# Kernel optimization log

Measured on AMD Instinct MI355X. Metric: run time of the kernel, lower is better.

Reference implementation:

```python
import jax, jax.numpy as jnp
from jax import lax
import numpy as np

WS = 8      # window_size
SS = 4      # shift_size
NH = 8      # num_heads
DIM = 192
HID = int(DIM * 2.66)  # 510


def _rel_pos_index(ws):
    coords = np.stack(np.meshgrid(np.arange(ws), np.arange(ws), indexing='ij'))
    flat = coords.reshape(2, -1)
    rel = (flat[:, :, None] - flat[:, None, :]).transpose(1, 2, 0)
    rel[..., 0] += ws - 1
    rel[..., 1] += ws - 1
    rel[..., 0] *= 2 * ws - 1
    return rel.sum(-1)  # (ws*ws, ws*ws) int


def _attn_mask(Hp, Wp, ws, ss):
    img = np.zeros((Hp, Wp), dtype=np.float32)
    slices = (slice(0, -ws), slice(-ws, -ss), slice(-ss, None))
    cnt = 0
    for h in slices:
        for w in slices:
            img[h, w] = cnt
            cnt += 1
    mw = img.reshape(Hp // ws, ws, Wp // ws, ws).transpose(0, 2, 1, 3).reshape(-1, ws * ws)
    am = mw[:, None, :] - mw[:, :, None]
    return np.where(am != 0, -100.0, 0.0).astype(np.float32)  # (nW, N, N)


def _ln(t, w, b):
    mu = t.mean(-1, keepdims=True)
    var = t.var(-1, keepdims=True)
    return (t - mu) / jnp.sqrt(var + 1e-5) * w + b


def setup_inputs() -> dict:
    key = jax.random.key(0)
    ks = jax.random.split(key, 12)
    s = 0.05
    return {
        'x': jax.random.normal(ks[0], (2, DIM, 256, 256), jnp.float32),
        'norm1_w': jnp.ones((DIM,), jnp.float32),
        'norm1_b': jnp.zeros((DIM,), jnp.float32),
        'qkv_w': jax.random.normal(ks[1], (3 * DIM, DIM), jnp.float32) * s,
        'rpb_table': jax.random.normal(ks[2], ((2 * WS - 1) * (2 * WS - 1), NH), jnp.float32) * 0.02,
        'proj_w': jax.random.normal(ks[3], (DIM, DIM), jnp.float32) * s,
        'proj_b': jnp.zeros((DIM,), jnp.float32),
        'norm2_w': jnp.ones((DIM,), jnp.float32),
        'norm2_b': jnp.zeros((DIM,), jnp.float32),
        'pin_w': jax.random.normal(ks[4], (2 * HID, DIM), jnp.float32) * s,
        'dw_w': jax.random.normal(ks[5], (2 * HID, 1, 3, 3), jnp.float32) * s,
        'pout_w': jax.random.normal(ks[6], (DIM, HID), jnp.float32) * s,
    }


def reference(x, norm1_w, norm1_b, qkv_w, rpb_table, proj_w, proj_b,
              norm2_w, norm2_b, pin_w, dw_w, pout_w):
    B, C, H, W = x.shape
    hd = C // NH
    scale = hd ** -0.5

    # ---- norm1 (channel-last layernorm) ----
    xc = jnp.transpose(x, (0, 2, 3, 1))  # BHWC
    xn = _ln(xc, norm1_w, norm1_b)

    # ---- pad to window multiple ----
    pad_b = (WS - H % WS) % WS
    pad_r = (WS - W % WS) % WS
    xn = jnp.pad(xn, ((0, 0), (0, pad_b), (0, pad_r), (0, 0)))
    Hp, Wp = H + pad_b, W + pad_r

    # ---- cyclic shift ----
    sx = jnp.roll(xn, (-SS, -SS), axis=(1, 2))

    # ---- window partition ----
    nH, nW = Hp // WS, Wp // WS
    N = WS * WS
    xw = sx.reshape(B, nH, WS, nW, WS, C).transpose(0, 1, 3, 2, 4, 5)
    xw = xw.reshape(B * nH * nW, N, C)

    # ---- window attention ----
    qkv = (xw @ qkv_w.T).reshape(-1, N, 3, NH, hd).transpose(2, 0, 3, 1, 4)
    q, k, v = qkv[0] * scale, qkv[1], qkv[2]  # (B_, NH, N, hd)
    attn = jnp.einsum('bhnd,bhmd->bhnm', q, k)

    idx = _rel_pos_index(WS)
    bias = rpb_table[idx.reshape(-1)].reshape(N, N, NH).transpose(2, 0, 1)
    attn = attn + bias[None]

    mask = jnp.asarray(_attn_mask(Hp, Wp, WS, SS))  # (nWtot, N, N)
    nWtot = nH * nW
    attn = attn.reshape(B, nWtot, NH, N, N) + mask[None, :, None]
    attn = jax.nn.softmax(attn.reshape(-1, NH, N, N), axis=-1)

    out = jnp.einsum('bhnm,bhmd->bhnd', attn, v)
    out = out.transpose(0, 2, 1, 3).reshape(-1, N, C)
    out = out @ proj_w.T + proj_b

    # ---- window reverse + unshift + crop ----
    out = out.reshape(B, nH, nW, WS, WS, C).transpose(0, 1, 3, 2, 4, 5)
    out = out.reshape(B, Hp, Wp, C)
    out = jnp.roll(out, (SS, SS), axis=(1, 2))[:, :H, :W]
    x = x + jnp.transpose(out, (0, 3, 1, 2))

    # ---- FFN: 1x1 in -> depthwise 3x3 -> gated gelu -> 1x1 out ----
    y = _ln(jnp.transpose(x, (0, 2, 3, 1)), norm2_w, norm2_b)
    y = jnp.transpose(y, (0, 3, 1, 2))
    y = jnp.einsum('bchw,oc->bohw', y, pin_w)
    y = lax.conv_general_dilated(y, dw_w, (1, 1), 'SAME',
                                 feature_group_count=dw_w.shape[0],
                                 dimension_numbers=('NCHW', 'OIHW', 'NCHW'))
    h = dw_w.shape[0] // 2
    y = jax.nn.gelu(y[:, :h], approximate=False) * y[:, h:]
    y = jnp.einsum('bchw,oc->bohw', y, pout_w)
    return x + y
```

## Files before the change

### kernel.cpp

```cpp
#include <hip/hip_runtime.h>
#include <hip/hip_bf16.h>
#include <math.h>

#define CDIM 192
#define NTOK 131072
#define HD 24
#define NHEADS 8
#define NTC 65536

typedef __attribute__((ext_vector_type(4))) float floatx4;
typedef __attribute__((ext_vector_type(8))) short bf16x8;
typedef __attribute__((ext_vector_type(4))) unsigned int uintx4;

static __device__ __forceinline__ float bf2f(__hip_bfloat16 h) { return __bfloat162float(h); }
static __device__ __forceinline__ __hip_bfloat16 f2bf(float f) { return __float2bfloat16(f); }
static __device__ __forceinline__ float s2f(short s) {
  union { unsigned u; float f; } c; c.u = ((unsigned)(unsigned short)s) << 16; return c.f;
}
static __device__ __forceinline__ short f2s(float f) {
  __hip_bfloat16 h = __float2bfloat16(f);
  union { __hip_bfloat16 h; short s; } c; c.h = h; return c.s;
}
static __device__ __forceinline__ void load_lds16(const void* g, void* l) {
  __builtin_amdgcn_global_load_lds(
      (const __attribute__((address_space(1))) void*)g,
      (__attribute__((address_space(3))) void*)l, 16, 0, 0);
}

__global__ __launch_bounds__(256) void kcvt(
    const float* __restrict__ in, __hip_bfloat16* __restrict__ out, int n) {
  int i = blockIdx.x * 256 + threadIdx.x;
  if (i < n) out[i] = f2bf(in[i]);
}

__global__ __launch_bounds__(256) void k0_padpout(
    const float* __restrict__ w, __hip_bfloat16* __restrict__ o) {
  int idx = blockIdx.x * 256 + threadIdx.x;
  int n = idx >> 9, k = idx & 511;
  o[idx] = (k < 510) ? f2bf(w[n * 510 + k]) : f2bf(0.f);
}

__global__ __launch_bounds__(256) void k0_padpin(
    const float* __restrict__ w, const float* __restrict__ nw,
    __hip_bfloat16* __restrict__ o) {
  int idx = blockIdx.x * 256 + threadIdx.x;
  int n = idx / 192, k = idx % 192;
  int src = (n < 510) ? n : ((n >= 512 && n < 1022) ? n - 2 : -1);
  o[idx] = (src >= 0) ? f2bf(w[src * 192 + k] * nw[k]) : f2bf(0.f);
}

__global__ __launch_bounds__(256) void k0_st(
    const float* __restrict__ w, const float* __restrict__ nw,
    const float* __restrict__ nb, float* __restrict__ S, float* __restrict__ T) {
  int n = blockIdx.x * 256 + threadIdx.x;
  int src = (n < 510) ? n : ((n >= 512 && n < 1022) ? n - 2 : -1);
  float s = 0.f, t = 0.f;
  if (src >= 0)
    for (int c = 0; c < 192; ++c) {
      float v = w[src * 192 + c];
      s += v * nw[c]; t += v * nb[c];
    }
  S[n] = s; T[n] = t;
}

__global__ __launch_bounds__(256) void k0_wtap(
    const float* __restrict__ wdw, __hip_bfloat16* __restrict__ wa,
    __hip_bfloat16* __restrict__ wg) {
  int idx = blockIdx.x * 256 + threadIdx.x;
  if (idx >= 9 * 512) return;
  int tap = idx >> 9, c = idx & 511;
  wa[idx] = (c < 510) ? f2bf(wdw[c * 9 + tap]) : f2bf(0.f);
  wg[idx] = (c < 510) ? f2bf(wdw[(c + 510) * 9 + tap]) : f2bf(0.f);
}

__global__ __launch_bounds__(256) void k1_ln_raster(
    const float* __restrict__ x,
    const float* __restrict__ w,
    const float* __restrict__ bsh,
    __hip_bfloat16* __restrict__ out) {
  __shared__ float xs[32][193];
  __shared__ float wls[192], bls[192];
  int bid = blockIdx.x;
  int b = bid >> 11, si = (bid >> 3) & 255, sj0 = (bid & 7) << 5;
  int i = (si + 4) & 255;
  int tid = threadIdx.x;
  int lane = tid & 63, wv = tid >> 6;
  if (tid < 192) { wls[tid] = w[tid]; bls[tid] = bsh[tid]; }
  int p0 = (lane & 7) << 2;
  int cb = wv * 8 + (lane >> 3);
  int j4 = (sj0 + p0 + 4) & 255;
  long pbase = ((long)(b * CDIM + cb) << 16) + (i << 8) + j4;
  #pragma unroll
  for (int co = 0; co < 6; ++co) {
    floatx4 v = *(const floatx4*)(x + pbase + ((long)co << 21));
    int c = co * 32 + cb;
    xs[p0 + 0][c] = v[0];
    xs[p0 + 1][c] = v[1];
    xs[p0 + 2][c] = v[2];
    xs[p0 + 3][c] = v[3];
  }
  __syncthreads();
  int p = tid >> 3, q = tid & 7, c0 = q * 24;
  float v[24], s = 0.f, sq = 0.f;
  #pragma unroll
  for (int e = 0; e < 24; ++e) {
    float t = xs[p][c0 + e]; v[e] = t; s += t; sq += t * t;
  }
  #pragma unroll
  for (int off = 1; off < 8; off <<= 1) { s += __shfl_xor(s, off); sq += __shfl_xor(sq, off); }
  float mean = s * (1.0f / 192.0f);
  float var  = sq * (1.0f / 192.0f) - mean * mean;
  float rstd = rsqrtf(var + 1e-5f);
  unsigned pk[12];
  #pragma unroll
  for (int e = 0; e < 12; ++e) {
    unsigned lo = (unsigned short)f2s((v[2*e  ] - mean) * rstd * wls[c0 + 2*e  ] + bls[c0 + 2*e  ]);
    unsigned hi = (unsigned short)f2s((v[2*e+1] - mean) * rstd * wls[c0 + 2*e+1] + bls[c0 + 2*e+1]);
    pk[e] = lo | (hi << 16);
  }
  long tok0 = ((long)b << 16) + (si << 8) + sj0;
  char* gout = (char*)out + (tok0 + p) * 384 + q * 48;
  *(uintx4*)(gout     ) = (uintx4){pk[0], pk[1], pk[2], pk[3]};
  *(uintx4*)(gout + 16) = (uintx4){pk[4], pk[5], pk[6], pk[7]};
  *(uintx4*)(gout + 32) = (uintx4){pk[8], pk[9], pk[10], pk[11]};
}

template <int WM, int WN, int EPI>
__global__ __launch_bounds__(256) void gemm_lds(
    const __hip_bfloat16* __restrict__ A,
    const __hip_bfloat16* __restrict__ B,
    const float* __restrict__ bias,
    __hip_bfloat16* __restrict__ C,
    int K, int lda, int ldb, int ldc) {
  constexpr int BM = 32 * WM, BN = 32 * WN;
  __shared__ __hip_bfloat16 As[BM * 32];
  __shared__ __hip_bfloat16 Bs[BN * 32];
  int t = threadIdx.x;
  int wave = t >> 6, lane = t & 63;
  int wm = wave >> 1, wn = wave & 1;
  int r16 = lane & 15, quad = lane >> 4;
  long m0 = (long)blockIdx.y * BM;
  long n0 = (long)blockIdx.x * BN;
  int srow = t >> 2, scol = (t & 3) << 3;
  floatx4 acc[WM][WN];
  for (int i = 0; i < WM; ++i)
    for (int j = 0; j < WN; ++j)
      acc[i][j] = (floatx4){0.f, 0.f, 0.f, 0.f};
  for (int k0 = 0; k0 < K; k0 += 32) {
    __syncthreads();
    for (int p = 0; p < WM / 2; ++p)
      load_lds16(A + (m0 + srow + p * 64) * lda + k0 + scol,
                 (char*)As + t * 16 + p * 4096);
    for (int p = 0; p < WN / 2; ++p)
      load_lds16(B + (n0 + srow + p * 64) * ldb + k0 + scol,
                 (char*)Bs + t * 16 + p * 4096);
    __syncthreads();
    bf16x8 af[WM], bf[WN];
    for (int i = 0; i < WM; ++i)
      af[i] = *(const bf16x8*)&As[(wm * 16 * WM + i * 16 + r16) * 32 + quad * 8];
    for (int j = 0; j < WN; ++j)
      bf[j] = *(const bf16x8*)&Bs[(wn * 16 * WN + j * 16 + r16) * 32 + quad * 8];
    for (int i = 0; i < WM; ++i)
      for (int j = 0; j < WN; ++j)
        acc[i][j] = __builtin_amdgcn_mfma_f32_16x16x32_bf16(af[i], bf[j], acc[i][j], 0, 0, 0);
  }
  for (int i = 0; i < WM; ++i)
    for (int j = 0; j < WN; ++j) {
      int col = n0 + wn * 16 * WN + j * 16 + r16;
      float badd = (EPI == 1) ? bias[col] : 0.f;
      for (int r = 0; r < 4; ++r) {
        long row = m0 + wm * 16 * WM + i * 16 + quad * 4 + r;
        C[row * ldc + col] = f2bf(acc[i][j][r] + badd);
      }
    }
}

__global__ __launch_bounds__(256) void gemm_qkv(
    const __hip_bfloat16* __restrict__ A,
    const __hip_bfloat16* __restrict__ B,
    __hip_bfloat16* __restrict__ C) {
  constexpr int WM = 4, WN = 2, BM = 128, BN = 64;
  __shared__ __hip_bfloat16 As[BM * 32];
  __shared__ __hip_bfloat16 Bs[BN * 32];
  int t = threadIdx.x;
  int wave = t >> 6, lane = t & 63;
  int wm = wave >> 1, wn = wave & 1;
  int r16 = lane & 15, quad = lane >> 4;
  long m0 = (long)blockIdx.y * BM;
  int n0 = blockIdx.x * BN;
  int srow = t >> 2, scol = (t & 3) << 3;
  floatx4 acc[WM][WN];
  for (int i = 0; i < WM; ++i)
    for (int j = 0; j < WN; ++j)
      acc[i][j] = (floatx4){0.f, 0.f, 0.f, 0.f};
  for (int k0 = 0; k0 < 192; k0 += 32) {
    __syncthreads();
    for (int p = 0; p < 2; ++p)
      load_lds16(A + (m0 + srow + p * 64) * 192 + k0 + scol,
                 (char*)As + t * 16 + p * 4096);
    load_lds16(B + (n0 + srow) * 192 + k0 + scol, (char*)Bs + t * 16);
    __syncthreads();
    bf16x8 af[WM], bf[WN];
    for (int i = 0; i < WM; ++i)
      af[i] = *(const bf16x8*)&As[(wm * 64 + i * 16 + r16) * 32 + quad * 8];
    for (int j = 0; j < WN; ++j)
      bf[j] = *(const bf16x8*)&Bs[(wn * 32 + j * 16 + r16) * 32 + quad * 8];
    for (int i = 0; i < WM; ++i)
      for (int j = 0; j < WN; ++j)
        acc[i][j] = __builtin_amdgcn_mfma_f32_16x16x32_bf16(af[i], bf[j], acc[i][j], 0, 0, 0);
  }
  for (int i = 0; i < WM; ++i)
    for (int j = 0; j < WN; ++j) {
      int col = n0 + wn * 32 + j * 16 + r16;
      int sel = col / 192;
      int cm = col - sel * 192;
      int h = (cm * 683) >> 14;
      int d = cm - h * 24;
      long cb = (long)sel * (NTC * 256) + ((long)h << 21) + d;
      for (int r = 0; r < 4; ++r) {
        long row = m0 + wm * 64 + i * 16 + quad * 4 + r;
        C[cb + (row << 5)] = f2bf(acc[i][j][r]);
      }
    }
}

__global__ __launch_bounds__(256) void gemm_pin(
    const __hip_bfloat16* __restrict__ x2,
    const __hip_bfloat16* __restrict__ B,
    const float* __restrict__ stats,
    const float* __restrict__ Sv,
    const float* __restrict__ Tv,
    __hip_bfloat16* __restrict__ C,
    int bb, int r0) {
  constexpr int WM = 4, WN = 4, BM = 128, BN = 128;
  __shared__ __hip_bfloat16 As[BM * 32];
  __shared__ __hip_bfloat16 Bs[BN * 32];
  int t = threadIdx.x;
  int wave = t >> 6, lane = t & 63;
  int wm = wave >> 1, wn = wave & 1;
  int r16 = lane & 15, quad = lane >> 4;
  int m0 = blockIdx.y * BM;
  int n0 = blockIdx.x * BN;
  int srow = t >> 2, scol = (t & 3) << 3;
  floatx4 acc[WM][WN];
  for (int i = 0; i < WM; ++i)
    for (int j = 0; j < WN; ++j)
      acc[i][j] = (floatx4){0.f, 0.f, 0.f, 0.f};
  for (int k0 = 0; k0 < 192; k0 += 32) {
    __syncthreads();
    for (int p = 0; p < 2; ++p) {
      int rr = m0 + srow + p * 64;
      int il = rr >> 8, jj = rr & 255;
      int gi = r0 - 1 + il; gi = gi < 0 ? 0 : (gi > 255 ? 255 : gi);
      long tok = ((long)bb << 16) + (gi << 8) + jj;
      load_lds16(x2 + tok * 192 + k0 + scol, (char*)As + t * 16 + p * 4096);
    }
    for (int p = 0; p < 2; ++p)
      load_lds16(B + (n0 + srow + p * 64) * 192 + k0 + scol,
                 (char*)Bs + t * 16 + p * 4096);
    __syncthreads();
    bf16x8 af[WM], bf[WN];
    for (int i = 0; i < WM; ++i)
      af[i] = *(const bf16x8*)&As[(wm * 64 + i * 16 + r16) * 32 + quad * 8];
    for (int j = 0; j < WN; ++j)
      bf[j] = *(const bf16x8*)&Bs[(wn * 64 + j * 16 + r16) * 32 + quad * 8];
    for (int i = 0; i < WM; ++i)
      for (int j = 0; j < WN; ++j)
        acc[i][j] = __builtin_amdgcn_mfma_f32_16x16x32_bf16(af[i], bf[j], acc[i][j], 0, 0, 0);
  }
  for (int i = 0; i < WM; ++i) {
    float mr[4], rsd[4];
    #pragma unroll
    for (int r = 0; r < 4; ++r) {
      int row = m0 + wm * 64 + i * 16 + quad * 4 + r;
      int il = row >> 8, jj = row & 255;
      int gi = r0 - 1 + il; gi = gi < 0 ? 0 : (gi > 255 ? 255 : gi);
      long tok = ((long)bb << 16) + (gi << 8) + jj;
      mr[r] = stats[2 * tok]; rsd[r] = stats[2 * tok + 1];
    }
    for (int j = 0; j < WN; ++j) {
      int col = n0 + wn * 64 + j * 16 + r16;
      float sv = Sv[col], tv = Tv[col];
      for (int r = 0; r < 4; ++r) {
        int row = m0 + wm * 64 + i * 16 + quad * 4 + r;
        C[(long)row * 1024 + col] = f2bf(acc[i][j][r] * rsd[r] - mr[r] * rsd[r] * sv + tv);
      }
    }
  }
}

__global__ __launch_bounds__(256) void gemm_pout(
    const __hip_bfloat16* __restrict__ A,
    const __hip_bfloat16* __restrict__ B,
    const __hip_bfloat16* __restrict__ x2,
    float* __restrict__ out,
    int b, int r0) {
  constexpr int WM = 2, WN = 4, BM = 64, BN = 128;
  __shared__ __hip_bfloat16 As[BM * 32];
  __shared__ __hip_bfloat16 Bs[BN * 32];
  int t = threadIdx.x;
  int wave = t >> 6, lane = t & 63;
  int wm = wave >> 1, wn = wave & 1;
  int r16 = lane & 15, quad = lane >> 4;
  long m0 = (long)blockIdx.y * BM;
  long n0 = (long)blockIdx.x * BN;
  int srow = t >> 2, scol = (t & 3) << 3;
  floatx4 acc[WM][WN];
  for (int i = 0; i < WM; ++i)
    for (int j = 0; j < WN; ++j)
      acc[i][j] = (floatx4){0.f, 0.f, 0.f, 0.f};
  for (int k0 = 0; k0 < 512; k0 += 32) {
    __syncthreads();
    load_lds16(A + (m0 + srow) * 512 + k0 + scol, (char*)As + t * 16);
    for (int p = 0; p < WN / 2; ++p)
      load_lds16(B + (n0 + srow + p * 64) * 512 + k0 + scol,
                 (char*)Bs + t * 16 + p * 4096);
    __syncthreads();
    bf16x8 af[WM], bf[WN];
    for (int i = 0; i < WM; ++i)
      af[i] = *(const bf16x8*)&As[(wm * 16 * WM + i * 16 + r16) * 32 + quad * 8];
    for (int j = 0; j < WN; ++j)
      bf[j] = *(const bf16x8*)&Bs[(wn * 16 * WN + j * 16 + r16) * 32 + quad * 8];
    for (int i = 0; i < WM; ++i)
      for (int j = 0; j < WN; ++j)
        acc[i][j] = __builtin_amdgcn_mfma_f32_16x16x32_bf16(af[i], bf[j], acc[i][j], 0, 0, 0);
  }
  for (int i = 0; i < WM; ++i)
    for (int j = 0; j < WN; ++j) {
      int p_ = n0 + wn * 16 * WN + j * 16 + r16;
      int il = p_ >> 8, jj = p_ & 255;
      long pix = ((long)(r0 + il) << 8) + jj;
      for (int r = 0; r < 4; ++r) {
        int c_ = m0 + wm * 16 * WM + i * 16 + quad * 4 + r;
        long tok = ((long)b << 16) + pix;
        float v = acc[i][j][r] + bf2f(x2[tok * CDIM + c_]);
        out[((long)(b * CDIM + c_) << 16) + pix] = v;
      }
    }
}

__global__ __launch_bounds__(256) void k3_attn(
    const __hip_bfloat16* __restrict__ qkv,
    const float* __restrict__ rpb,
    __hip_bfloat16* __restrict__ out,
    int wid0) {
  __shared__ alignas(16) short Kp[64 * 32];
  __shared__ alignas(16) short Vt[32 * 64];
  __shared__ alignas(16) short Ps[4][16 * 64];
  __shared__ float rpbs[225];
  int h = blockIdx.x, widl = blockIdx.y;
  int wid = wid0 + widl;
  int t = threadIdx.x;
  int wv = t >> 6, lane = t & 63, quad = lane >> 4, r16 = lane & 15;
  int wi_l = widl >> 5, wjl = widl & 31;
  const short* qk = (const short*)qkv;
  const short* Qp  = qk + ((long)h << 21);
  const short* Kpg = Qp + (long)NTC * 256;
  const short* Vpg = Qp + (long)NTC * 512;

  if (t < 225) rpbs[t] = rpb[t * NHEADS + h];

  {
    int kr = t >> 2, kq = t & 3;
    bf16x8 kv = {0, 0, 0, 0, 0, 0, 0, 0};
    if (kq < 3) {
      int ltok = ((((wi_l << 3) + (kr >> 3)) << 8) + (wjl << 3) + (kr & 7));
      kv = *(const bf16x8*)(Kpg + ((long)ltok << 5) + kq * 8);
    }
    *(bf16x8*)&Kp[kr * 32 + ((kq ^ ((kr >> 1) & 3)) << 3)] = kv;
  }
  {
    int tok = t & 63, q8 = t >> 6;
    if (q8 < 3) {
      int ltok = ((((wi_l << 3) + (tok >> 3)) << 8) + (wjl << 3) + (tok & 7));
      bf16x8 vv = *(const bf16x8*)(Vpg + ((long)ltok << 5) + q8 * 8);
      #pragma unroll
      for (int e = 0; e < 8; ++e) {
        int d = q8 * 8 + e;
        Vt[d * 64 + (((tok >> 3) ^ (d & 7)) << 3) + (tok & 7)] = vv[e];
      }
    } else {
      int zt = t - 192;
      int d = 24 + (zt >> 3), tokg = zt & 7;
      bf16x8 z = {0, 0, 0, 0, 0, 0, 0, 0};
      *(bf16x8*)&Vt[d * 64 + ((tokg ^ (d & 7)) << 3)] = z;
    }
  }
  bf16x8 qf = {0, 0, 0, 0, 0, 0, 0, 0};
  if (quad < 3) {
    int nn = wv * 16 + r16;
    int ltok = ((((wi_l << 3) + (nn >> 3)) << 8) + (wjl << 3) + (nn & 7));
    qf = *(const bf16x8*)(Qp + ((long)ltok << 5) + quad * 8);
  }
  __syncthreads();

  floatx4 sj[4];
  int kswz = (quad ^ ((r16 >> 1) & 3)) << 3;
  #pragma unroll
  for (int j = 0; j < 4; ++j) {
    bf16x8 kf = *(const bf16x8*)&Kp[(j * 16 + r16) * 32 + kswz];
    sj[j] = __builtin_amdgcn_mfma_f32_16x16x32_bf16(
        qf, kf, (floatx4){0.f, 0.f, 0.f, 0.f}, 0, 0, 0);
  }

  int b = wid >> 10, wi = (wid >> 5) & 31, wj = wid & 31;
  int rkj[4];
  #pragma unroll
  for (int j = 0; j < 4; ++j) {
    int m = j * 16 + r16;
    int gsi = wi * 8 + (m >> 3), gsj = wj * 8 + (m & 7);
    rkj[j] = ((gsi < 248) ? 0 : (gsi < 252 ? 1 : 2)) * 3 +
             ((gsj < 248) ? 0 : (gsj < 252 ? 1 : 2));
  }

  float rs[4];
  #pragma unroll
  for (int r = 0; r < 4; ++r) {
    int n = wv * 16 + quad * 4 + r;
    int ti = n >> 3, tj = n & 7;
    int gi = wi * 8 + ti, gj = wj * 8 + tj;
    int rq = ((gi < 248) ? 0 : (gi < 252 ? 1 : 2)) * 3 +
             ((gj < 248) ? 0 : (gj < 252 ? 1 : 2));
    float val[4];
    float mx = -1e30f;
    #pragma unroll
    for (int j = 0; j < 4; ++j) {
      int m = j * 16 + r16;
      int idx = (ti - (m >> 3) + 7) * 15 + (tj - (m & 7) + 7);
      float v = sj[j][r] * 0.20412414523193154f + rpbs[idx];
      if (rkj[j] != rq) v -= 100.0f;
      val[j] = v;
      mx = fmaxf(mx, v);
    }
    #pragma unroll
    for (int off = 1; off < 16; off <<= 1) mx = fmaxf(mx, __shfl_xor(mx, off));
    float sum = 0.f;
    int row = quad * 4 + r;
    #pragma unroll
    for (int j = 0; j < 4; ++j) {
      float p = __expf(val[j] - mx);
      sum += p;
      int col = j * 16 + r16;
      Ps[wv][row * 64 + ((((col >> 3) ^ (row & 7)) << 3)) + (col & 7)] = f2s(p);
    }
    #pragma unroll
    for (int off = 1; off < 16; off <<= 1) sum += __shfl_xor(sum, off);
    rs[r] = 1.0f / sum;
  }
  __syncthreads();

  floatx4 o0 = {0.f, 0.f, 0.f, 0.f}, o1 = {0.f, 0.f, 0.f, 0.f};
  #pragma unroll
  for (int kk = 0; kk < 2; ++kk) {
    int g = (((kk * 4 + quad) ^ (r16 & 7)) << 3);
    bf16x8 pa = *(const bf16x8*)&Ps[wv][r16 * 64 + g];
    bf16x8 b0 = *(const bf16x8*)&Vt[r16 * 64 + g];
    bf16x8 b1 = *(const bf16x8*)&Vt[(16 + r16) * 64 + g];
    o0 = __builtin_amdgcn_mfma_f32_16x16x32_bf16(pa, b0, o0, 0, 0, 0);
    o1 = __builtin_amdgcn_mfma_f32_16x16x32_bf16(pa, b1, o1, 0, 0, 0);
  }
  #pragma unroll
  for (int r = 0; r < 4; ++r) {
    int n = wv * 16 + quad * 4 + r;
    int gi = wi * 8 + (n >> 3), gj = wj * 8 + (n & 7);
    long ob = (((long)b << 16) + (gi << 8) + gj) * CDIM + h * HD;
    out[ob + r16] = f2bf(o0[r] * rs[r]);
    if (r16 < 8) out[ob + 16 + r16] = f2bf(o1[r] * rs[r]);
  }
}

__global__ __launch_bounds__(256) void k4_res_raster(
    const float* __restrict__ x,
    const __hip_bfloat16* __restrict__ tmp,
    __hip_bfloat16* __restrict__ x2,
    float* __restrict__ stats) {
  __shared__ float xs[32][193];
  int bid = blockIdx.x;
  int b = bid >> 11, i = (bid >> 3) & 255, j0 = (bid & 7) << 5;
  int tid = threadIdx.x;
  int lane = tid & 63, wv = tid >> 6;
  int p0 = (lane & 7) << 2;
  int cb = wv * 8 + (lane >> 3);
  long pbase = ((long)(b * CDIM + cb) << 16) + (i << 8) + j0 + p0;
  #pragma unroll
  for (int co = 0; co < 6; ++co) {
    floatx4 v = *(const floatx4*)(x + pbase + ((long)co << 21));
    int c = co * 32 + cb;
    xs[p0 + 0][c] = v[0];
    xs[p0 + 1][c] = v[1];
    xs[p0 + 2][c] = v[2];
    xs[p0 + 3][c] = v[3];
  }
  __syncthreads();
  int p = tid >> 3, q = tid & 7, c0 = q * 24;
  int j = j0 + p;
  int si = (i + 252) & 255, sj = (j + 252) & 255;
  long tsh = ((long)b << 16) + (si << 8) + sj;
  const short* tp = (const short*)tmp + tsh * 192 + c0;
  bf16x8 t0 = *(const bf16x8*)(tp);
  bf16x8 t1 = *(const bf16x8*)(tp + 8);
  bf16x8 t2v = *(const bf16x8*)(tp + 16);
  float v[24], s = 0.f, sq = 0.f;
  #pragma unroll
  for (int e = 0; e < 8; ++e) {
    float a0 = xs[p][c0 + e     ] + s2f(t0[e]);
    float a1 = xs[p][c0 + e + 8 ] + s2f(t1[e]);
    float a2 = xs[p][c0 + e + 16] + s2f(t2v[e]);
    v[e] = a0; v[e + 8] = a1; v[e + 16] = a2;
    s += a0 + a1 + a2;
    sq += a0 * a0 + a1 * a1 + a2 * a2;
  }
  #pragma unroll
  for (int off = 1; off < 8; off <<= 1) { s += __shfl_xor(s, off); sq += __shfl_xor(sq, off); }
  float mean = s * (1.0f / 192.0f);
  float var  = sq * (1.0f / 192.0f) - mean * mean;
  float rstd = rsqrtf(var + 1e-5f);
  long t2g = ((long)b << 16) + (i << 8) + j;
  if (q == 0) { stats[2 * t2g] = mean; stats[2 * t2g + 1] = rstd; }
  unsigned pk[12];
  #pragma unroll
  for (int e = 0; e < 12; ++e) {
    unsigned lo = (unsigned short)f2s(v[2 * e]);
    unsigned hi = (unsigned short)f2s(v[2 * e + 1]);
    pk[e] = lo | (hi << 16);
  }
  char* gout = (char*)x2 + t2g * 384 + q * 48;
  *(uintx4*)(gout     ) = (uintx4){pk[0], pk[1], pk[2], pk[3]};
  *(uintx4*)(gout + 16) = (uintx4){pk[4], pk[5], pk[6], pk[7]};
  *(uintx4*)(gout + 32) = (uintx4){pk[8], pk[9], pk[10], pk[11]};
}

__global__ __launch_bounds__(256) void k7_dwgate(
    const __hip_bfloat16* __restrict__ pin,
    const __hip_bfloat16* __restrict__ wa,
    const __hip_bfloat16* __restrict__ wg,
    __hip_bfloat16* __restrict__ out,
    int r0) {
  int t = threadIdx.x;
  int oct = t & 63, pl = t >> 6;
  int p = blockIdx.x * 4 + pl;
  int il = p >> 8, j = p & 255;
  int gi = r0 + il;
  int c0 = oct << 3;
  float a[8], g[8];
  for (int e = 0; e < 8; ++e) { a[e] = 0.f; g[e] = 0.f; }
  for (int di = -1; di <= 1; ++di) {
    int ii = gi + di; if (ii < 0 || ii > 255) continue;
    int br = il + di + 1;
    for (int dj = -1; dj <= 1; ++dj) {
      int jj = j + dj; if (jj < 0 || jj > 255) continue;
      long nbase = ((long)((br << 8) + jj)) << 10;
      int tap = (di + 1) * 3 + (dj + 1);
      bf16x8 va  = *(const bf16x8*)((const short*)pin + nbase + c0);
      bf16x8 vg  = *(const bf16x8*)((const short*)pin + nbase + 512 + c0);
      bf16x8 wa8 = *(const bf16x8*)((const short*)wa + tap * 512 + c0);
      bf16x8 wg8 = *(const bf16x8*)((const short*)wg + tap * 512 + c0);
      for (int e = 0; e < 8; ++e) {
        a[e] += s2f(wa8[e]) * s2f(va[e]);
        g[e] += s2f(wg8[e]) * s2f(vg[e]);
      }
    }
  }
  bf16x8 r;
  for (int e = 0; e < 8; ++e) {
    float ge = 0.5f * a[e] * (1.0f + erff(a[e] * 0.70710678118654752f));
    r[e] = f2s(ge * g[e]);
  }
  *(bf16x8*)((short*)out + (long)p * 512 + c0) = r;
}

extern "C" void kernel_launch(void* const* d_in, const int* in_sizes, int n_in,
                              void* d_out, int out_size, void* d_ws, size_t ws_size,
                              hipStream_t stream) {
  const float* x       = (const float*)d_in[0];
  const float* norm1_w = (const float*)d_in[1];
  const float* norm1_b = (const float*)d_in[2];
  const float* qkv_w   = (const float*)d_in[3];
  const float* rpb     = (const float*)d_in[4];
  const float* proj_w  = (const float*)d_in[5];
  const float* proj_b  = (const float*)d_in[6];
  const float* norm2_w = (const float*)d_in[7];
  const float* norm2_b = (const float*)d_in[8];
  const float* pin_w   = (const float*)d_in[9];
  const float* dw_w    = (const float*)d_in[10];
  const float* pout_w  = (const float*)d_in[11];

  char* ws = (char*)d_ws;
  __hip_bfloat16* wsLN1 = (__hip_bfloat16*)(ws);
  __hip_bfloat16* wsPRJ = (__hip_bfloat16*)(ws);
  __hip_bfloat16* wsPINC= (__hip_bfloat16*)(ws);
  __hip_bfloat16* wsATT = (__hip_bfloat16*)(ws + 50331648UL);
  __hip_bfloat16* wsX2  = (__hip_bfloat16*)(ws + 50331648UL);
  float*          wsST  = (float*)         (ws + 100663296UL);
  __hip_bfloat16* wsGT  = (__hip_bfloat16*)(ws + 101711872UL);
  __hip_bfloat16* wsWA  = (__hip_bfloat16*)(ws + 118489088UL);
  __hip_bfloat16* wsWG  = (__hip_bfloat16*)(ws + 118507520UL);
  float*          wsS   = (float*)         (ws + 118517760UL);
  float*          wsT   = (float*)         (ws + 118525952UL);
  __hip_bfloat16* wsPW  = (__hip_bfloat16*)(ws + 120586240UL);
  __hip_bfloat16* wsQW  = (__hip_bfloat16*)(ws + 120782848UL);
  __hip_bfloat16* wsPJW = (__hip_bfloat16*)(ws + 121004032UL);
  __hip_bfloat16* wsPIW = (__hip_bfloat16*)(ws + 121077760UL);
  float* out = (float*)d_out;
  __hip_bfloat16* qkvbuf = (__hip_bfloat16*)d_out;

  kcvt<<<(110592 + 255) / 256, 256, 0, stream>>>(qkv_w, wsQW, 110592);
  kcvt<<<(36864 + 255) / 256, 256, 0, stream>>>(proj_w, wsPJW, 36864);
  k0_padpout<<<384, 256, 0, stream>>>(pout_w, wsPW);
  k0_padpin<<<768, 256, 0, stream>>>(pin_w, norm2_w, wsPIW);
  k0_st<<<4, 256, 0, stream>>>(pin_w, norm2_w, norm2_b, wsS, wsT);
  k0_wtap<<<18, 256, 0, stream>>>(dw_w, wsWA, wsWG);
  k1_ln_raster<<<4096, 256, 0, stream>>>(x, norm1_w, norm1_b, wsLN1);
  for (int b = 0; b < 2; ++b) {
    gemm_qkv<<<dim3(9, 512), 256, 0, stream>>>(
        wsLN1 + (long)b * 65536 * CDIM, wsQW, qkvbuf);
    k3_attn<<<dim3(8, 1024), 256, 0, stream>>>(qkvbuf, rpb, wsATT, b * 1024);
  }
  gemm_lds<4, 2, 1><<<dim3(3, 1024), 256, 0, stream>>>(
      wsATT, wsPJW, proj_b, wsPRJ, 192, 192, 192, 192);
  k4_res_raster<<<4096, 256, 0, stream>>>(x, wsPRJ, wsX2, wsST);
  for (int cc = 0; cc < 8; ++cc) {
    int b = cc >> 2, r0 = (cc & 3) * 64;
    gemm_pin<<<dim3(8, 132), 256, 0, stream>>>(
        wsX2, wsPIW, wsST, wsS, wsT, wsPINC, b, r0);
    k7_dwgate<<<4096, 256, 0, stream>>>(wsPINC, wsWA, wsWG, wsGT, r0);
    gemm_pout<<<dim3(128, 3), 256, 0, stream>>>(wsPW, wsGT, wsX2, out, b, r0);
  }
}
```

Measured before the change: 929.7 us.

## Store QKV token-major via generic GEMM and group attention blocks by window

Drops the custom QKV GEMM that scattered output into a head-major padded layout. The generic GEMM now writes a plain token-major 576-wide row, and the attention kernel reads Q/K/V slices at per-head offsets. The attention grid becomes 1D, with blocks remapped so the eight heads of a group of windows run next to each other for better cache locality. The GEMM stores become contiguous, but attention loads now use a larger stride (48-byte pieces out of 1152-byte rows).

```diff
diff --git a/kernel.cpp b/kernel.cpp
--- a/kernel.cpp
+++ b/kernel.cpp
@@ -175,55 +175,6 @@
     }
 }
 
-__global__ __launch_bounds__(256) void gemm_qkv(
-    const __hip_bfloat16* __restrict__ A,
-    const __hip_bfloat16* __restrict__ B,
-    __hip_bfloat16* __restrict__ C) {
-  constexpr int WM = 4, WN = 2, BM = 128, BN = 64;
-  __shared__ __hip_bfloat16 As[BM * 32];
-  __shared__ __hip_bfloat16 Bs[BN * 32];
-  int t = threadIdx.x;
-  int wave = t >> 6, lane = t & 63;
-  int wm = wave >> 1, wn = wave & 1;
-  int r16 = lane & 15, quad = lane >> 4;
-  long m0 = (long)blockIdx.y * BM;
-  int n0 = blockIdx.x * BN;
-  int srow = t >> 2, scol = (t & 3) << 3;
-  floatx4 acc[WM][WN];
-  for (int i = 0; i < WM; ++i)
-    for (int j = 0; j < WN; ++j)
-      acc[i][j] = (floatx4){0.f, 0.f, 0.f, 0.f};
-  for (int k0 = 0; k0 < 192; k0 += 32) {
-    __syncthreads();
-    for (int p = 0; p < 2; ++p)
-      load_lds16(A + (m0 + srow + p * 64) * 192 + k0 + scol,
-                 (char*)As + t * 16 + p * 4096);
-    load_lds16(B + (n0 + srow) * 192 + k0 + scol, (char*)Bs + t * 16);
-    __syncthreads();
-    bf16x8 af[WM], bf[WN];
-    for (int i = 0; i < WM; ++i)
-      af[i] = *(const bf16x8*)&As[(wm * 64 + i * 16 + r16) * 32 + quad * 8];
-    for (int j = 0; j < WN; ++j)
-      bf[j] = *(const bf16x8*)&Bs[(wn * 32 + j * 16 + r16) * 32 + quad * 8];
-    for (int i = 0; i < WM; ++i)
-      for (int j = 0; j < WN; ++j)
-        acc[i][j] = __builtin_amdgcn_mfma_f32_16x16x32_bf16(af[i], bf[j], acc[i][j], 0, 0, 0);
-  }
-  for (int i = 0; i < WM; ++i)
-    for (int j = 0; j < WN; ++j) {
-      int col = n0 + wn * 32 + j * 16 + r16;
-      int sel = col / 192;
-      int cm = col - sel * 192;
-      int h = (cm * 683) >> 14;
-      int d = cm - h * 24;
-      long cb = (long)sel * (NTC * 256) + ((long)h << 21) + d;
-      for (int r = 0; r < 4; ++r) {
-        long row = m0 + wm * 64 + i * 16 + quad * 4 + r;
-        C[cb + (row << 5)] = f2bf(acc[i][j][r]);
-      }
-    }
-}
-
 __global__ __launch_bounds__(256) void gemm_pin(
     const __hip_bfloat16* __restrict__ x2,
     const __hip_bfloat16* __restrict__ B,
@@ -348,15 +299,14 @@
   __shared__ alignas(16) short Vt[32 * 64];
   __shared__ alignas(16) short Ps[4][16 * 64];
   __shared__ float rpbs[225];
-  int h = blockIdx.x, widl = blockIdx.y;
+  int bidx = blockIdx.x;
+  int h = (bidx >> 3) & 7;
+  int widl = ((bidx >> 6) << 3) | (bidx & 7);
   int wid = wid0 + widl;
   int t = threadIdx.x;
   int wv = t >> 6, lane = t & 63, quad = lane >> 4, r16 = lane & 15;
   int wi_l = widl >> 5, wjl = widl & 31;
   const short* qk = (const short*)qkv;
-  const short* Qp  = qk + ((long)h << 21);
-  const short* Kpg = Qp + (long)NTC * 256;
-  const short* Vpg = Qp + (long)NTC * 512;
 
   if (t < 225) rpbs[t] = rpb[t * NHEADS + h];
 
@@ -364,16 +314,16 @@
     int kr = t >> 2, kq = t & 3;
     bf16x8 kv = {0, 0, 0, 0, 0, 0, 0, 0};
     if (kq < 3) {
-      int ltok = ((((wi_l << 3) + (kr >> 3)) << 8) + (wjl << 3) + (kr & 7));
-      kv = *(const bf16x8*)(Kpg + ((long)ltok << 5) + kq * 8);
+      long ltok = (long)((((wi_l << 3) + (kr >> 3)) << 8) + (wjl << 3) + (kr & 7));
+      kv = *(const bf16x8*)(qk + ltok * 576 + 192 + h * HD + kq * 8);
     }
     *(bf16x8*)&Kp[kr * 32 + ((kq ^ ((kr >> 1) & 3)) << 3)] = kv;
   }
   {
     int tok = t & 63, q8 = t >> 6;
     if (q8 < 3) {
-      int ltok = ((((wi_l << 3) + (tok >> 3)) << 8) + (wjl << 3) + (tok & 7));
-      bf16x8 vv = *(const bf16x8*)(Vpg + ((long)ltok << 5) + q8 * 8);
+      long ltok = (long)((((wi_l << 3) + (tok >> 3)) << 8) + (wjl << 3) + (tok & 7));
+      bf16x8 vv = *(const bf16x8*)(qk + ltok * 576 + 384 + h * HD + q8 * 8);
       #pragma unroll
       for (int e = 0; e < 8; ++e) {
         int d = q8 * 8 + e;
@@ -389,8 +339,8 @@
   bf16x8 qf = {0, 0, 0, 0, 0, 0, 0, 0};
   if (quad < 3) {
     int nn = wv * 16 + r16;
-    int ltok = ((((wi_l << 3) + (nn >> 3)) << 8) + (wjl << 3) + (nn & 7));
-    qf = *(const bf16x8*)(Qp + ((long)ltok << 5) + quad * 8);
+    long ltok = (long)((((wi_l << 3) + (nn >> 3)) << 8) + (wjl << 3) + (nn & 7));
+    qf = *(const bf16x8*)(qk + ltok * 576 + h * HD + quad * 8);
   }
   __syncthreads();
 
@@ -612,9 +562,9 @@
   k0_wtap<<<18, 256, 0, stream>>>(dw_w, wsWA, wsWG);
   k1_ln_raster<<<4096, 256, 0, stream>>>(x, norm1_w, norm1_b, wsLN1);
   for (int b = 0; b < 2; ++b) {
-    gemm_qkv<<<dim3(9, 512), 256, 0, stream>>>(
-        wsLN1 + (long)b * 65536 * CDIM, wsQW, qkvbuf);
-    k3_attn<<<dim3(8, 1024), 256, 0, stream>>>(qkvbuf, rpb, wsATT, b * 1024);
+    gemm_lds<4, 2, 0><<<dim3(9, 512), 256, 0, stream>>>(
+        wsLN1 + (long)b * 65536 * CDIM, wsQW, nullptr, qkvbuf, 192, 192, 192, 576);
+    k3_attn<<<8192, 256, 0, stream>>>(qkvbuf, rpb, wsATT, b * 1024);
   }
   gemm_lds<4, 2, 1><<<dim3(3, 1024), 256, 0, stream>>>(
       wsATT, wsPJW, proj_b, wsPRJ, 192, 192, 192, 192);
```

Result: faster. 890.0 us (-4.3%).
